# Kernel tuning notes

Measured on AMD Instinct MI355X. Metric: run time of the kernel, lower is better.

The kernel has to match this reference:

```python
import jax, jax.numpy as jnp
import numpy as np

B, S, D, NQ, NC, MC, K = 64, 200, 128, 50000, 1000, 4, 10
N = NQ + NC  # total graph nodes (concepts first, then questions, matching torch concat order)


def setup_inputs() -> dict:
    key = jax.random.key(0)
    ks = jax.random.split(key, 32)
    f = lambda i, shape: jax.random.normal(ks[i], shape, dtype=jnp.float32) * 0.02
    return {
        "emb_q": f(0, (NQ, D)), "emb_c": f(1, (NC, D)), "emb_r": f(2, (2, D)),
        "Wih1": f(3, (3 * D, 2 * D)), "Whh1": f(4, (3 * D, D)), "bih1": f(5, (3 * D,)), "bhh1": f(6, (3 * D,)),
        "Wih2": f(7, (3 * D, D)), "Whh2": f(8, (3 * D, D)), "bih2": f(9, (3 * D,)), "bhh2": f(10, (3 * D,)),
        "Wg1": f(11, (D, D)), "Wg2": f(12, (D, D)), "Wg3": f(13, (D, D)),
        "Wagg": f(14, (D, D)), "bagg": f(15, (D,)),
        "Wq": f(16, (D, D)), "bq": f(17, (D,)),
        "Wk": f(18, (D, D)), "bk": f(19, (D,)),
        "Ww": f(20, (1, 2 * D)), "bw": f(21, (1,)),
        "question_seq": jax.random.randint(ks[22], (B, S), 0, NQ),
        "correct_seq": jax.random.randint(ks[23], (B, S), 0, 2),
        "mask_seq": jnp.ones((B, S), dtype=jnp.int32),
        "q_table": jax.random.randint(ks[24], (NQ, MC), 0, NC),
    }


def _gru(x, h, Wih, Whh, bih, bhh):
    gi = x @ Wih.T + bih
    gh = h @ Whh.T + bhh
    i_r, i_z, i_n = jnp.split(gi, 3, axis=-1)
    h_r, h_z, h_n = jnp.split(gh, 3, axis=-1)
    r = jax.nn.sigmoid(i_r + h_r)
    z = jax.nn.sigmoid(i_z + h_z)
    n = jnp.tanh(i_n + r * h_n)
    return (1.0 - z) * n + z * h


def _sage_mean(x, src, dst, W):
    # SAGEConv4GIKT (eval): out = lin_r(mean_agg_over_neighbors + x), lin_r has no bias.
    agg = jax.ops.segment_sum(x[dst], src, num_segments=N)
    cnt = jax.ops.segment_sum(jnp.ones((src.shape[0], 1), x.dtype), src, num_segments=N)
    agg = agg / jnp.maximum(cnt, 1.0)
    return (agg + x) @ W.T


def reference(emb_q, emb_c, emb_r, Wih1, Whh1, bih1, bhh1, Wih2, Whh2, bih2, bhh2,
              Wg1, Wg2, Wg3, Wagg, bagg, Wq, bq, Wk, bk, Ww, bw,
              question_seq, correct_seq, mask_seq, q_table):
    # ---- GNN propagation over the full question-concept bipartite graph ----
    x = jnp.concatenate([emb_c, emb_q], axis=0)  # [N, D], concepts first
    q_glob = jnp.repeat(jnp.arange(NQ, dtype=q_table.dtype) + NC, MC)  # question global ids
    c_glob = q_table.reshape(-1)                                       # concept global ids
    x = _sage_mean(x, q_glob, c_glob, Wg1)  # q2c: aggregate at questions from concepts
    x = _sage_mean(x, c_glob, q_glob, Wg2)  # c2q: aggregate at concepts from questions
    x = _sage_mean(x, q_glob, c_glob, Wg3)  # q2c again
    x = jnp.tanh(x @ Wagg.T + bagg)

    tgrid = jnp.arange(S)

    def step(carry, inp):
        h1, h2, keyhist, statehist = carry
        t, q_t, r_t, m_t, q_next = inp
        m = (m_t != 0)[:, None]
        e_q = jnp.where(m, x[q_t + NC], emb_q[q_t])  # GNN emb where masked-in, raw emb otherwise
        e_r = emb_r[r_t]
        h1 = _gru(jnp.concatenate([e_q, e_r], axis=1), h1, Wih1, Whh1, bih1, bhh1)
        h2 = _gru(h1, h2, Wih2, Whh2, bih2, bhh2)
        statehist = statehist.at[:, t].set(h2)
        keyhist = keyhist.at[:, t].set(h2 @ Wk.T + bk)
        # queries: next question emb + its concept embs -> [B, MC+1, D]
        qc = jnp.concatenate([emb_q[q_next][:, None, :], emb_c[q_table[q_next]]], axis=1)
        aq = qc @ Wq.T + bq
        scores = jnp.einsum('bid,bjd->bij', aq, keyhist)  # [B, MC+1, S]
        scores = jnp.where((tgrid <= t)[None, None, :], scores, -1e9)
        flat = scores.reshape(B, -1)
        vals, idx = jax.lax.top_k(flat, K)  # top-k (query, state) pairs
        alpha = jax.nn.softmax(vals, axis=-1)
        i_idx = idx // S
        j_idx = idx % S
        q_sel = jnp.take_along_axis(qc, i_idx[:, :, None], axis=1)        # [B, K, D]
        s_sel = jnp.take_along_axis(statehist, j_idx[:, :, None], axis=1)  # [B, K, D]
        f = jax.nn.sigmoid(jnp.concatenate([q_sel, s_sel], axis=-1) @ Ww.T + bw)[..., 0]
        y = jnp.sum(alpha * f, axis=-1)  # [B]
        return (h1, h2, keyhist, statehist), y

    h0 = jnp.zeros((B, D), jnp.float32)
    carry = (h0, h0, jnp.zeros((B, S, D), jnp.float32), jnp.zeros((B, S, D), jnp.float32))
    xs = (jnp.arange(S - 1), question_seq[:, :-1].T, correct_seq[:, :-1].T,
          mask_seq[:, :-1].T, question_seq[:, 1:].T)
    _, ys = jax.lax.scan(step, carry, xs)
    y_hat = jnp.concatenate([jnp.zeros((B, 1), jnp.float32), ys.T], axis=1)  # predictions for t=1..S-1
    return y_hat
```

## Files before the change

kernel.cpp:

```cpp
#include <hip/hip_runtime.h>
#include <math.h>

#define Bz 64
#define Sz 200
#define Dz 128
#define NQz 50000
#define NCz 1000
#define MCz 4
#define Kz 10
#define Tz 199
#define NSz (Bz*Tz)
#define NEz (NQz*MCz)
#define KTpad 256

__global__ void k_count(const int* __restrict__ qt, int* __restrict__ cnt) {
    int e = blockIdx.x*256 + threadIdx.x;
    if (e < NEz) atomicAdd(&cnt[qt[e]], 1);
}

__global__ void k_offs(const int* __restrict__ cnt, int* __restrict__ offs) {
    __shared__ int s[1024];
    int tid = threadIdx.x;
    s[tid] = (tid < NCz) ? cnt[tid] : 0;
    __syncthreads();
    for (int off = 1; off < 1024; off <<= 1) {
        int add = (tid >= off) ? s[tid - off] : 0;
        __syncthreads();
        s[tid] += add;
        __syncthreads();
    }
    if (tid < NCz) offs[tid + 1] = s[tid];
    if (tid == 0) offs[0] = 0;
}

__global__ void k_fill(const int* __restrict__ qt, const int* __restrict__ offs,
                       int* __restrict__ fill, int* __restrict__ edge_q) {
    int e = blockIdx.x*256 + threadIdx.x;
    if (e < NEz) {
        int c = qt[e];
        int pos = atomicAdd(&fill[c], 1);
        edge_q[offs[c] + pos] = e >> 2;
    }
}

__global__ void k_m2(const int* __restrict__ qt, const int* __restrict__ offs,
                     const int* __restrict__ edge_q,
                     const float* __restrict__ emb_q, const float* __restrict__ emb_c,
                     float* __restrict__ m2) {
    int c = blockIdx.x;
    int g = threadIdx.x >> 7;
    int d = threadIdx.x & 127;
    int e0 = offs[c], e1 = offs[c+1];
    float acc = 0.f;
    for (int e = e0 + g; e < e1; e += 4) {
        int q = edge_q[e];
        const int* t4 = qt + q*4;
        int c0 = t4[0], c1 = t4[1], c2 = t4[2], c3 = t4[3];
        acc += emb_q[q*128 + d]
             + 0.25f*(emb_c[c0*128+d] + emb_c[c1*128+d] + emb_c[c2*128+d] + emb_c[c3*128+d]);
    }
    __shared__ float ps[4][128];
    ps[g][d] = acc;
    __syncthreads();
    if (g == 0) {
        float tot = ps[0][d] + ps[1][d] + ps[2][d] + ps[3][d];
        float cn = (float)(e1 - e0);
        m2[c*128 + d] = tot / fmaxf(cn, 1.0f);
    }
}

template<bool TR>
__global__ void k_mm128(const float* __restrict__ X, const float* __restrict__ Y,
                        float* __restrict__ out) {
    int r = blockIdx.x, c = threadIdx.x;
    float acc = 0.f;
    for (int e = 0; e < 128; ++e) acc += X[r*128 + e] * Y[e*128 + c];
    if (TR) out[c*128 + r] = acc;
    else    out[r*128 + c] = acc;
}

__global__ void k_gr(const float* __restrict__ emb_r, const float* __restrict__ Wih1,
                     const float* __restrict__ bih1, float* __restrict__ gr) {
    int rt = threadIdx.x / 384, r = threadIdx.x % 384;
    float acc = bih1[r];
    for (int e = 0; e < 128; ++e) acc += emb_r[rt*128 + e] * Wih1[r*256 + 128 + e];
    gr[rt*384 + r] = acc;
}

__global__ void k_bkq(const float* __restrict__ Wq, const float* __restrict__ Wk,
                      const float* __restrict__ bq, const float* __restrict__ bk,
                      const float* __restrict__ Ww, const float* __restrict__ bw,
                      float* __restrict__ Bkq, float* __restrict__ biaskq) {
    int r = blockIdx.x, d = threadIdx.x;
    if (r < 128) {
        float acc = 0.f;
        for (int n = 0; n < 128; ++n) acc += Wq[n*128 + r] * Wk[n*128 + d];
        Bkq[r*128 + d] = acc;
        if (d == 0) {
            float b0 = 0.f;
            for (int n = 0; n < 128; ++n) b0 += Wq[n*128 + r] * bk[n];
            biaskq[r] = b0;
        }
    } else if (r == 128) {
        float acc = 0.f;
        for (int n = 0; n < 128; ++n) acc += bq[n] * Wk[n*128 + d];
        Bkq[128*128 + d] = acc;
        if (d == 0) {
            float c0 = 0.f;
            for (int n = 0; n < 128; ++n) c0 += bq[n] * bk[n];
            biaskq[128] = c0;
        }
    } else {
        Bkq[129*128 + d] = Ww[128 + d];
        if (d == 0) biaskq[129] = bw[0];
    }
}

__global__ void k_eq(const float* __restrict__ Mt_g, const float* __restrict__ bagg,
                     const float* __restrict__ emb_q, const float* __restrict__ emb_c,
                     const float* __restrict__ m2, const int* __restrict__ qseq,
                     const int* __restrict__ mseq, const int* __restrict__ qt,
                     float* __restrict__ eq) {
    __shared__ float Mt[128*128];
    __shared__ float ub[2][128];
    int tid = threadIdx.x;
    for (int i = tid; i < 128*128/4; i += 256)
        ((float4*)Mt)[i] = ((const float4*)Mt_g)[i];
    __syncthreads();
    int g = tid >> 7, d = tid & 127;
    for (int it = 0; it < 8; ++it) {
        int slot = blockIdx.x*16 + it*2 + g;
        int b = slot / Tz, t = slot % Tz;
        int q = qseq[b*Sz + t];
        int msk = mseq[b*Sz + t];
        if (msk) {
            const int* t4 = qt + q*4;
            int c0 = t4[0], c1 = t4[1], c2 = t4[2], c3 = t4[3];
            ub[g][d] = emb_q[q*128 + d]
                     + 0.5f *(emb_c[c0*128+d] + emb_c[c1*128+d] + emb_c[c2*128+d] + emb_c[c3*128+d])
                     + 0.25f*(m2[c0*128+d]  + m2[c1*128+d]  + m2[c2*128+d]  + m2[c3*128+d]);
        }
        __syncthreads();
        if (msk) {
            float acc = bagg[d];
            const float* urow = ub[g];
            for (int e = 0; e < 128; ++e) acc += Mt[e*128 + d] * urow[e];
            eq[slot*128 + d] = tanhf(acc);
        } else {
            eq[slot*128 + d] = emb_q[q*128 + d];
        }
        __syncthreads();
    }
}

__device__ __forceinline__ float bf_lo(unsigned u){ return __uint_as_float(u << 16); }
__device__ __forceinline__ float bf_hi(unsigned u){ return __uint_as_float(u & 0xffff0000u); }
__device__ __forceinline__ unsigned f2bf(float x){
    unsigned u = __float_as_uint(x);
    return (u + 0x7fffu + ((u >> 16) & 1u)) >> 16;
}
__device__ __forceinline__ unsigned pk2(float a, float b){
    return f2bf(a) | (f2bf(b) << 16);
}
__device__ __forceinline__ float rcpf(float x){ return __builtin_amdgcn_rcpf(x); }
__device__ __forceinline__ float sigm(float x){ return rcpf(1.f + __expf(-x)); }
__device__ __forceinline__ float tanh_fast(float x){
    float e = __expf(2.f*x);
    return 1.f - 2.f*rcpf(e + 1.f);
}

#if __has_builtin(__builtin_amdgcn_fdot2_f32_bf16)
typedef __attribute__((ext_vector_type(2))) short short2v;
__device__ __forceinline__ float bdot2(unsigned w, unsigned h, float acc) {
    return __builtin_amdgcn_fdot2_f32_bf16(__builtin_bit_cast(short2v, w),
                                           __builtin_bit_cast(short2v, h), acc, false);
}
#else
__device__ __forceinline__ float bdot2(unsigned w, unsigned h, float acc) {
    return acc + bf_lo(w)*bf_lo(h) + bf_hi(w)*bf_hi(h);
}
#endif

typedef __attribute__((ext_vector_type(2))) float v2f;
__device__ __forceinline__ void pkfma_lo(v2f &acc, v2f k, v2f q) {
    asm("v_pk_fma_f32 %0, %1, %2, %0 op_sel_hi:[1,0,1]"
        : "+v"(acc) : "v"(k), "v"(q));
}
__device__ __forceinline__ void pkfma_hi(v2f &acc, v2f k, v2f q) {
    asm("v_pk_fma_f32 %0, %1, %2, %0 op_sel:[0,1,0] op_sel_hi:[1,1,1]"
        : "+v"(acc) : "v"(k), "v"(q));
}

template<int MODE, int DOT2>
__global__ void k_gemm(const float* __restrict__ A, const float* __restrict__ Bm,
                       int ldb, int nB, float* __restrict__ C, int ldc,
                       const float* __restrict__ bias, const float* __restrict__ gr,
                       const int* __restrict__ cseq) {
    __shared__ int rtb[64];
    int tx = threadIdx.x, ty = threadIdx.y;
    int tid = ty*16 + tx;
    int m0 = blockIdx.x * 64;
    int n0 = blockIdx.y * 64;
    if (MODE == 1 && tid < 64) {
        int s = m0 + tid;
        int b = s / Tz, t = s % Tz;
        rtb[tid] = cseq[b*Sz + t];
    }
    float acc[4][4];
    #pragma unroll
    for (int i = 0; i < 4; ++i)
        #pragma unroll
        for (int j = 0; j < 4; ++j) acc[i][j] = 0.f;

    if (DOT2) {
        __shared__ unsigned As[64][17];
        __shared__ unsigned Bs[64][17];
        for (int kc = 0; kc < 128; kc += 32) {
            #pragma unroll
            for (int l = 0; l < 2; ++l) {
                int v = tid*2 + l;
                int row = v >> 3, c4 = (v & 7) << 2;
                int p0 = (kc + c4) >> 1 & 15;
                float4 av = *(const float4*)(A + (size_t)(m0+row)*128 + kc + c4);
                As[row][p0]   = pk2(av.x, av.y);
                As[row][p0+1] = pk2(av.z, av.w);
                int nrow = n0 + row;
                float4 bv = make_float4(0.f, 0.f, 0.f, 0.f);
                if (nrow < nB) bv = *(const float4*)(Bm + (size_t)nrow*ldb + kc + c4);
                Bs[row][p0]   = pk2(bv.x, bv.y);
                Bs[row][p0+1] = pk2(bv.z, bv.w);
            }
            __syncthreads();
            #pragma unroll 4
            for (int kp = 0; kp < 16; ++kp) {
                unsigned av[4], bv[4];
                #pragma unroll
                for (int i = 0; i < 4; ++i) av[i] = As[ty*4+i][kp];
                #pragma unroll
                for (int j = 0; j < 4; ++j) bv[j] = Bs[tx*4+j][kp];
                #pragma unroll
                for (int i = 0; i < 4; ++i)
                    #pragma unroll
                    for (int j = 0; j < 4; ++j) acc[i][j] = bdot2(av[i], bv[j], acc[i][j]);
            }
            __syncthreads();
        }
    } else {
        __shared__ float Asf[64][33];
        __shared__ float Bsf[64][33];
        for (int kc = 0; kc < 128; kc += 32) {
            #pragma unroll
            for (int l = 0; l < 2; ++l) {
                int v = tid*2 + l;
                int row = v >> 3, c4 = (v & 7) << 2;
                float4 av = *(const float4*)(A + (size_t)(m0+row)*128 + kc + c4);
                Asf[row][c4+0] = av.x; Asf[row][c4+1] = av.y; Asf[row][c4+2] = av.z; Asf[row][c4+3] = av.w;
                int nrow = n0 + row;
                float4 bv = make_float4(0.f, 0.f, 0.f, 0.f);
                if (nrow < nB) bv = *(const float4*)(Bm + (size_t)nrow*ldb + kc + c4);
                Bsf[row][c4+0] = bv.x; Bsf[row][c4+1] = bv.y; Bsf[row][c4+2] = bv.z; Bsf[row][c4+3] = bv.w;
            }
            __syncthreads();
            #pragma unroll 8
            for (int k = 0; k < 32; ++k) {
                float av[4], bv[4];
                #pragma unroll
                for (int i = 0; i < 4; ++i) av[i] = Asf[ty*4+i][k];
                #pragma unroll
                for (int j = 0; j < 4; ++j) bv[j] = Bsf[tx*4+j][k];
                #pragma unroll
                for (int i = 0; i < 4; ++i)
                    #pragma unroll
                    for (int j = 0; j < 4; ++j) acc[i][j] += av[i]*bv[j];
            }
            __syncthreads();
        }
    }
    #pragma unroll
    for (int i = 0; i < 4; ++i) {
        int s = m0 + ty*4 + i;
        if (MODE == 2) {
            int bb = s / Tz, tt = s - ((int)(s / Tz))*Tz;
            #pragma unroll
            for (int j = 0; j < 4; ++j) {
                int col = n0 + tx*4 + j;
                if (col < nB)
                    C[((size_t)bb*132 + col)*KTpad + tt] = acc[i][j] + bias[col];
            }
        } else {
            #pragma unroll
            for (int j = 0; j < 4; ++j) {
                int col = n0 + tx*4 + j;
                if (col < nB) {
                    float v = acc[i][j];
                    if (MODE == 0) v += bias[col];
                    else           v += gr[rtb[ty*4+i]*384 + col];
                    C[(size_t)s*ldc + col] = v;
                }
            }
        }
    }
}

__global__ void __launch_bounds__(384, 1)
k_scan(const float* __restrict__ gi, const float* __restrict__ Whh,
       const float* __restrict__ bhh, float* __restrict__ hout) {
    int b0 = blockIdx.x*2, tid = threadIdx.x;

    unsigned w[64];
    {
        const float4* w4 = (const float4*)(Whh + (size_t)tid*128);
        #pragma unroll
        for (int k = 0; k < 32; ++k) {
            float4 v = w4[k];
            w[2*k] = pk2(v.x, v.y); w[2*k+1] = pk2(v.z, v.w);
        }
    }
    float bb = bhh[tid];

    __shared__ unsigned hb[2][64];
    __shared__ float gh[2][384];
    if (tid < 128) hb[tid>>6][tid&63] = 0u;

    float g0=0.f,g1=0.f,g2=0.f,g3=0.f,g4=0.f,g5=0.f;
    if (tid < 128) {
        const float2* gp = (const float2*)(gi + (size_t)((b0 + (tid>>6))*Tz)*384);
        int u = tid & 63;
        float2 x0 = gp[u], x1 = gp[u+64], x2 = gp[u+128];
        g0=x0.x; g1=x0.y; g2=x1.x; g3=x1.y; g4=x2.x; g5=x2.y;
    }
    __syncthreads();

    const uint4* hv0 = (const uint4*)hb[0];
    const uint4* hv1 = (const uint4*)hb[1];

    for (int t = 0; t < Tz; ++t) {
        float n0=0.f,n1=0.f,n2=0.f,n3=0.f,n4=0.f,n5=0.f;
        if (tid < 128 && t + 1 < Tz) {
            const float2* gp = (const float2*)(gi + (size_t)((b0 + (tid>>6))*Tz + t + 1)*384);
            int u = tid & 63;
            float2 x0 = gp[u], x1 = gp[u+64], x2 = gp[u+128];
            n0=x0.x; n1=x0.y; n2=x1.x; n3=x1.y; n4=x2.x; n5=x2.y;
        }
        float a0=0.f, a1=0.f, a2=0.f, a3=0.f;
        float c0=0.f, c1=0.f, c2=0.f, c3=0.f;
        #pragma unroll
        for (int k = 0; k < 8; ++k) {
            uint4 hp = hv0[k];
            uint4 hq = hv1[k];
            a0 = bdot2(w[4*k+0], hp.x, a0);
            a1 = bdot2(w[4*k+1], hp.y, a1);
            a2 = bdot2(w[4*k+2], hp.z, a2);
            a3 = bdot2(w[4*k+3], hp.w, a3);
            c0 = bdot2(w[4*k+0], hq.x, c0);
            c1 = bdot2(w[4*k+1], hq.y, c1);
            c2 = bdot2(w[4*k+2], hq.z, c2);
            c3 = bdot2(w[4*k+3], hq.w, c3);
        }
        gh[0][tid] = bb + ((a0+a1)+(a2+a3));
        gh[1][tid] = bb + ((c0+c1)+(c2+c3));
        __syncthreads();
        if (tid < 128) {
            int ch = tid >> 6;
            int u = 2*(tid & 63);
            unsigned hp = hb[ch][tid & 63];
            const float* ghc = gh[ch];
            float r0 = sigm(g0 + ghc[u]);
            float r1 = sigm(g1 + ghc[u+1]);
            float z0 = sigm(g2 + ghc[u+128]);
            float z1 = sigm(g3 + ghc[u+129]);
            float q0 = tanh_fast(g4 + r0*ghc[u+256]);
            float q1 = tanh_fast(g5 + r1*ghc[u+257]);
            float h0  = (1.f - z0)*q0 + z0*bf_lo(hp);
            float h1v = (1.f - z1)*q1 + z1*bf_hi(hp);
            hb[ch][tid & 63] = pk2(h0, h1v);
            ((float2*)(hout + (size_t)((b0+ch)*Tz + t)*128))[tid & 63] = make_float2(h0, h1v);
        }
        g0=n0; g1=n1; g2=n2; g3=n3; g4=n4; g5=n5;
        __syncthreads();
    }
}

__global__ void __launch_bounds__(256, 1)
k_attn(const float* __restrict__ kqt, const int* __restrict__ qseq,
       const int* __restrict__ qt, const float* __restrict__ emb_q,
       const float* __restrict__ emb_c, const float* __restrict__ Ww,
       float* __restrict__ out) {
    int wid  = threadIdx.x >> 6;
    int lane = threadIdx.x & 63;
    int b = blockIdx.y;
    int t = blockIdx.x*4 + wid;
    if (t > Tz - 1) t = Tz - 1;

    __shared__ float qc[4][5][128];
    __shared__ float gqs[4][5];
    int qn = qseq[b*Sz + t + 1];
    for (int idx = lane; idx < 5*128; idx += 64) {
        int i = idx / 128, d = idx & 127;
        const float* src = (i == 0) ? (emb_q + (size_t)qn*128)
                                    : (emb_c + (size_t)qt[qn*4 + (i-1)]*128);
        qc[wid][i][d] = src[d];
    }
    __syncthreads();
    {
        float w0 = Ww[lane], w1 = Ww[lane + 64];
        #pragma unroll
        for (int i = 0; i < 5; ++i) {
            float p = qc[wid][i][lane]*w0 + qc[wid][i][lane+64]*w1;
            #pragma unroll
            for (int off = 32; off >= 1; off >>= 1) p += __shfl_xor(p, off);
            if (lane == 0) gqs[wid][i] = p;
        }
    }
    __syncthreads();

    const float* base = kqt + (size_t)b*(132*KTpad);

    v2f accA[5], accB[5];
    #pragma unroll
    for (int i = 0; i < 5; ++i) { accA[i] = (v2f){0.f,0.f}; accB[i] = (v2f){0.f,0.f}; }

    #pragma unroll 2
    for (int c = 0; c < 32; ++c) {
        float4 k0 = ((const float4*)(base + (size_t)(4*c+0)*KTpad))[lane];
        float4 k1 = ((const float4*)(base + (size_t)(4*c+1)*KTpad))[lane];
        float4 k2 = ((const float4*)(base + (size_t)(4*c+2)*KTpad))[lane];
        float4 k3 = ((const float4*)(base + (size_t)(4*c+3)*KTpad))[lane];
        v2f k0a = {k0.x,k0.y}, k0b = {k0.z,k0.w};
        v2f k1a = {k1.x,k1.y}, k1b = {k1.z,k1.w};
        v2f k2a = {k2.x,k2.y}, k2b = {k2.z,k2.w};
        v2f k3a = {k3.x,k3.y}, k3b = {k3.z,k3.w};
        #pragma unroll
        for (int i = 0; i < 5; ++i) {
            float4 q = ((const float4*)qc[wid][i])[c];
            v2f qa = {q.x,q.y}, qb = {q.z,q.w};
            pkfma_lo(accA[i], k0a, qa); pkfma_lo(accB[i], k0b, qa);
            pkfma_hi(accA[i], k1a, qa); pkfma_hi(accB[i], k1b, qa);
            pkfma_lo(accA[i], k2a, qb); pkfma_lo(accB[i], k2b, qb);
            pkfma_hi(accA[i], k3a, qb); pkfma_hi(accB[i], k3b, qb);
        }
    }

    const float NEG = -3.402823466e38f;
    float sv[10]; int si[10];
    #pragma unroll
    for (int k = 0; k < 10; ++k) { sv[k] = NEG; si[k] = 0x7FFFFFFF; }

    auto ins = [&](float cv, int ci) {
        if (cv > sv[9] || (cv == sv[9] && ci < si[9])) {
            #pragma unroll
            for (int k = 0; k < 10; ++k) {
                bool bet = (cv > sv[k]) || (cv == sv[k] && ci < si[k]);
                float tv = sv[k]; int ti = si[k];
                if (bet) { sv[k] = cv; si[k] = ci; cv = tv; ci = ti; }
            }
        }
    };
    {
        float4 kb4 = ((const float4*)(base + 128*KTpad))[lane];
        float kbv[4] = {kb4.x, kb4.y, kb4.z, kb4.w};
        #pragma unroll
        for (int jj = 0; jj < 4; ++jj) {
            int j = 4*lane + jj;
            if (j <= t) {
                #pragma unroll
                for (int i = 0; i < 5; ++i) {
                    float a = (jj == 0) ? accA[i].x : (jj == 1) ? accA[i].y
                            : (jj == 2) ? accB[i].x : accB[i].y;
                    ins(a + kbv[jj], i*Sz + j);
                }
            }
        }
    }

    float vmax = 0.f, myv = 0.f; int myidx = 0x7FFFFFFF;
    #pragma unroll
    for (int rnd = 0; rnd < 10; ++rnd) {
        float v = sv[0]; int idx = si[0];
        #pragma unroll
        for (int off = 32; off >= 1; off >>= 1) {
            float ov = __shfl_xor(v, off);
            int   oi = __shfl_xor(idx, off);
            if (ov > v || (ov == v && oi < idx)) { v = ov; idx = oi; }
        }
        if (rnd == 0) vmax = v;
        if (lane == rnd) { myv = v; myidx = idx; }
        if (si[0] == idx) {
            #pragma unroll
            for (int k = 0; k < 9; ++k) { sv[k] = sv[k+1]; si[k] = si[k+1]; }
            sv[9] = NEG; si[9] = 0x7FFFFFFF;
        }
    }

    float num = 0.f, den = 0.f;
    if (lane < 10 && myidx != 0x7FFFFFFF) {
        float a = __expf(myv - vmax);
        int ik = myidx / Sz, jk = myidx % Sz;
        float gsj = base[129*KTpad + jk];
        float f = sigm(gqs[wid][ik] + gsj);
        num = a*f; den = a;
    }
    #pragma unroll
    for (int off = 32; off >= 1; off >>= 1) {
        num += __shfl_xor(num, off);
        den += __shfl_xor(den, off);
    }
    if (lane == 0) out[b*Sz + t + 1] = num/den;
}

static inline size_t alup(size_t x) { return (x + 255) & ~(size_t)255; }

extern "C" void kernel_launch(void* const* d_in, const int* in_sizes, int n_in,
                              void* d_out, int out_size, void* d_ws, size_t ws_size,
                              hipStream_t stream) {
    (void)in_sizes; (void)n_in; (void)ws_size;
    const float* emb_q = (const float*)d_in[0];
    const float* emb_c = (const float*)d_in[1];
    const float* emb_r = (const float*)d_in[2];
    const float* Wih1  = (const float*)d_in[3];
    const float* Whh1  = (const float*)d_in[4];
    const float* bih1  = (const float*)d_in[5];
    const float* bhh1  = (const float*)d_in[6];
    const float* Wih2  = (const float*)d_in[7];
    const float* Whh2  = (const float*)d_in[8];
    const float* bih2  = (const float*)d_in[9];
    const float* bhh2  = (const float*)d_in[10];
    const float* Wg1   = (const float*)d_in[11];
    const float* Wg2   = (const float*)d_in[12];
    const float* Wg3   = (const float*)d_in[13];
    const float* Wagg  = (const float*)d_in[14];
    const float* bagg  = (const float*)d_in[15];
    const float* Wq    = (const float*)d_in[16];
    const float* bq    = (const float*)d_in[17];
    const float* Wk    = (const float*)d_in[18];
    const float* bk    = (const float*)d_in[19];
    const float* Ww    = (const float*)d_in[20];
    const float* bw    = (const float*)d_in[21];
    const int* qseq    = (const int*)d_in[22];
    const int* cseq    = (const int*)d_in[23];
    const int* mseq    = (const int*)d_in[24];
    const int* qtab    = (const int*)d_in[25];
    float* out = (float*)d_out;

    char* p = (char*)d_ws;
    auto alloc = [&](size_t bytes) { char* r = p; p += alup(bytes); return r; };
    int*   cnt    = (int*)  alloc(4096);
    int*   fill   = (int*)  alloc(4096);
    int*   offs   = (int*)  alloc(1001*4);
    int*   edge_q = (int*)  alloc((size_t)NEz*4);
    float* m2     = (float*)alloc((size_t)NCz*128*4);
    float* T1     = (float*)alloc(128*128*4);
    float* T2     = (float*)alloc(128*128*4);
    float* Mt     = (float*)alloc(128*128*4);
    float* gr     = (float*)alloc(2*384*4);
    float* Bkq    = (float*)alloc(132*128*4);
    float* biaskq = (float*)alloc(132*4);
    float* eq     = (float*)alloc((size_t)NSz*128*4);
    float* gi1    = (float*)alloc((size_t)NSz*384*4);
    float* stateh = (float*)alloc((size_t)NSz*128*4);
    float* kqt    = (float*)alloc((size_t)Bz*132*KTpad*4);
    float* h1all = eq;
    float* gi2   = gi1;

    hipMemsetAsync(cnt, 0, 8192, stream);
    hipMemsetAsync(d_out, 0, (size_t)out_size*4, stream);

    k_count<<<(NEz+255)/256, 256, 0, stream>>>(qtab, cnt);
    k_offs <<<1, 1024, 0, stream>>>(cnt, offs);
    k_fill <<<(NEz+255)/256, 256, 0, stream>>>(qtab, offs, fill, edge_q);
    k_m2   <<<NCz, 512, 0, stream>>>(qtab, offs, edge_q, emb_q, emb_c, m2);

    k_mm128<false><<<128, 128, 0, stream>>>(Wg2, Wg1, T1);
    k_mm128<false><<<128, 128, 0, stream>>>(Wg3, T1, T2);
    k_mm128<true> <<<128, 128, 0, stream>>>(Wagg, T2, Mt);
    k_gr  <<<1, 768, 0, stream>>>(emb_r, Wih1, bih1, gr);
    k_bkq <<<130, 128, 0, stream>>>(Wq, Wk, bq, bk, Ww, bw, Bkq, biaskq);

    k_eq  <<<NSz/16, 256, 0, stream>>>(Mt, bagg, emb_q, emb_c, m2, qseq, mseq, qtab, eq);

    k_gemm<1,1><<<dim3(NSz/64, 6), dim3(16,16), 0, stream>>>(eq, Wih1, 256, 384,
                                                             gi1, 384, nullptr, gr, cseq);
    k_scan<<<Bz/2, 384, 0, stream>>>(gi1, Whh1, bhh1, h1all);
    k_gemm<0,1><<<dim3(NSz/64, 6), dim3(16,16), 0, stream>>>(h1all, Wih2, 128, 384,
                                                             gi2, 384, bih2, nullptr, nullptr);
    k_scan<<<Bz/2, 384, 0, stream>>>(gi2, Whh2, bhh2, stateh);

    k_gemm<2,0><<<dim3(NSz/64, 3), dim3(16,16), 0, stream>>>(stateh, Bkq, 128, 132,
                                                             kqt, 0, biaskq, nullptr, nullptr);
    k_attn<<<dim3((Tz+3)/4, Bz), 256, 0, stream>>>(kqt, qseq, qtab, emb_q, emb_c, Ww, out);
}
```

Baseline: 718.9 us.

## Restructure GRU scan to one batch per block with split-K shuffle reduction

After: 695.3 us. 3.3% less time.

```diff
diff --git a/kernel.cpp b/kernel.cpp
--- a/kernel.cpp
+++ b/kernel.cpp
@@ -302,81 +302,97 @@
     }
 }
 
-__global__ void __launch_bounds__(384, 1)
+__global__ void __launch_bounds__(512, 1)
 k_scan(const float* __restrict__ gi, const float* __restrict__ Whh,
        const float* __restrict__ bhh, float* __restrict__ hout) {
-    int b0 = blockIdx.x*2, tid = threadIdx.x;
-
-    unsigned w[64];
+    int b = blockIdx.x, tid = threadIdx.x;
+    int wid = tid >> 6, lane = tid & 63;
+    int u  = wid*16 + (lane & 15);
+    int qh = lane >> 4;
+
+    unsigned wr[16], wz[16], wn[16];
     {
-        const float4* w4 = (const float4*)(Whh + (size_t)tid*128);
-        #pragma unroll
-        for (int k = 0; k < 32; ++k) {
-            float4 v = w4[k];
-            w[2*k] = pk2(v.x, v.y); w[2*k+1] = pk2(v.z, v.w);
-        }
-    }
-    float bb = bhh[tid];
-
-    __shared__ unsigned hb[2][64];
-    __shared__ float gh[2][384];
-    if (tid < 128) hb[tid>>6][tid&63] = 0u;
-
-    float g0=0.f,g1=0.f,g2=0.f,g3=0.f,g4=0.f,g5=0.f;
-    if (tid < 128) {
-        const float2* gp = (const float2*)(gi + (size_t)((b0 + (tid>>6))*Tz)*384);
-        int u = tid & 63;
-        float2 x0 = gp[u], x1 = gp[u+64], x2 = gp[u+128];
-        g0=x0.x; g1=x0.y; g2=x1.x; g3=x1.y; g4=x2.x; g5=x2.y;
-    }
-    __syncthreads();
-
-    const uint4* hv0 = (const uint4*)hb[0];
-    const uint4* hv1 = (const uint4*)hb[1];
-
-    for (int t = 0; t < Tz; ++t) {
-        float n0=0.f,n1=0.f,n2=0.f,n3=0.f,n4=0.f,n5=0.f;
-        if (tid < 128 && t + 1 < Tz) {
-            const float2* gp = (const float2*)(gi + (size_t)((b0 + (tid>>6))*Tz + t + 1)*384);
-            int u = tid & 63;
-            float2 x0 = gp[u], x1 = gp[u+64], x2 = gp[u+128];
-            n0=x0.x; n1=x0.y; n2=x1.x; n3=x1.y; n4=x2.x; n5=x2.y;
-        }
-        float a0=0.f, a1=0.f, a2=0.f, a3=0.f;
-        float c0=0.f, c1=0.f, c2=0.f, c3=0.f;
+        const float4* r4 = (const float4*)(Whh + (size_t)u*128       + qh*32);
+        const float4* z4 = (const float4*)(Whh + (size_t)(u+128)*128 + qh*32);
+        const float4* n4 = (const float4*)(Whh + (size_t)(u+256)*128 + qh*32);
         #pragma unroll
         for (int k = 0; k < 8; ++k) {
-            uint4 hp = hv0[k];
-            uint4 hq = hv1[k];
-            a0 = bdot2(w[4*k+0], hp.x, a0);
-            a1 = bdot2(w[4*k+1], hp.y, a1);
-            a2 = bdot2(w[4*k+2], hp.z, a2);
-            a3 = bdot2(w[4*k+3], hp.w, a3);
-            c0 = bdot2(w[4*k+0], hq.x, c0);
-            c1 = bdot2(w[4*k+1], hq.y, c1);
-            c2 = bdot2(w[4*k+2], hq.z, c2);
-            c3 = bdot2(w[4*k+3], hq.w, c3);
-        }
-        gh[0][tid] = bb + ((a0+a1)+(a2+a3));
-        gh[1][tid] = bb + ((c0+c1)+(c2+c3));
-        __syncthreads();
-        if (tid < 128) {
-            int ch = tid >> 6;
-            int u = 2*(tid & 63);
-            unsigned hp = hb[ch][tid & 63];
-            const float* ghc = gh[ch];
-            float r0 = sigm(g0 + ghc[u]);
-            float r1 = sigm(g1 + ghc[u+1]);
-            float z0 = sigm(g2 + ghc[u+128]);
-            float z1 = sigm(g3 + ghc[u+129]);
-            float q0 = tanh_fast(g4 + r0*ghc[u+256]);
-            float q1 = tanh_fast(g5 + r1*ghc[u+257]);
-            float h0  = (1.f - z0)*q0 + z0*bf_lo(hp);
-            float h1v = (1.f - z1)*q1 + z1*bf_hi(hp);
-            hb[ch][tid & 63] = pk2(h0, h1v);
-            ((float2*)(hout + (size_t)((b0+ch)*Tz + t)*128))[tid & 63] = make_float2(h0, h1v);
-        }
-        g0=n0; g1=n1; g2=n2; g3=n3; g4=n4; g5=n5;
+            float4 a = r4[k]; wr[2*k] = pk2(a.x, a.y); wr[2*k+1] = pk2(a.z, a.w);
+            float4 c = z4[k]; wz[2*k] = pk2(c.x, c.y); wz[2*k+1] = pk2(c.z, c.w);
+            float4 d = n4[k]; wn[2*k] = pk2(d.x, d.y); wn[2*k+1] = pk2(d.z, d.w);
+        }
+    }
+    float br = bhh[u], bz = bhh[u+128], bn = bhh[u+256];
+
+    __shared__ unsigned hb[2][64];
+    if (tid < 64) { hb[0][tid] = 0u; hb[1][tid] = 0u; }
+    float hold = 0.f;
+
+    const float* gbase = gi + (size_t)(b*Tz)*384;
+    float gc0 = gbase[u], gc1 = gbase[u+128], gc2 = gbase[u+256];
+    float ga0 = gbase[384+u], ga1 = gbase[384+u+128], ga2 = gbase[384+u+256];
+    __syncthreads();
+
+    for (int t = 0; t < Tz; ++t) {
+        float gm0 = 0.f, gm1 = 0.f, gm2 = 0.f;
+        if (t + 2 < Tz) {
+            const float* gp = gbase + (size_t)(t+2)*384;
+            gm0 = gp[u]; gm1 = gp[u+128]; gm2 = gp[u+256];
+        }
+        const unsigned* hc = hb[t & 1];
+        const uint4* hv = (const uint4*)(hc + qh*16);
+        uint4 h0 = hv[0], h1 = hv[1], h2 = hv[2], h3 = hv[3];
+        float ar, az, an;
+        {
+            float p0=0.f, p1=0.f;
+            p0 = bdot2(wr[0],  h0.x, p0); p1 = bdot2(wr[1],  h0.y, p1);
+            p0 = bdot2(wr[2],  h0.z, p0); p1 = bdot2(wr[3],  h0.w, p1);
+            p0 = bdot2(wr[4],  h1.x, p0); p1 = bdot2(wr[5],  h1.y, p1);
+            p0 = bdot2(wr[6],  h1.z, p0); p1 = bdot2(wr[7],  h1.w, p1);
+            p0 = bdot2(wr[8],  h2.x, p0); p1 = bdot2(wr[9],  h2.y, p1);
+            p0 = bdot2(wr[10], h2.z, p0); p1 = bdot2(wr[11], h2.w, p1);
+            p0 = bdot2(wr[12], h3.x, p0); p1 = bdot2(wr[13], h3.y, p1);
+            p0 = bdot2(wr[14], h3.z, p0); p1 = bdot2(wr[15], h3.w, p1);
+            ar = p0 + p1;
+        }
+        {
+            float p0=0.f, p1=0.f;
+            p0 = bdot2(wz[0],  h0.x, p0); p1 = bdot2(wz[1],  h0.y, p1);
+            p0 = bdot2(wz[2],  h0.z, p0); p1 = bdot2(wz[3],  h0.w, p1);
+            p0 = bdot2(wz[4],  h1.x, p0); p1 = bdot2(wz[5],  h1.y, p1);
+            p0 = bdot2(wz[6],  h1.z, p0); p1 = bdot2(wz[7],  h1.w, p1);
+            p0 = bdot2(wz[8],  h2.x, p0); p1 = bdot2(wz[9],  h2.y, p1);
+            p0 = bdot2(wz[10], h2.z, p0); p1 = bdot2(wz[11], h2.w, p1);
+            p0 = bdot2(wz[12], h3.x, p0); p1 = bdot2(wz[13], h3.y, p1);
+            p0 = bdot2(wz[14], h3.z, p0); p1 = bdot2(wz[15], h3.w, p1);
+            az = p0 + p1;
+        }
+        {
+            float p0=0.f, p1=0.f;
+            p0 = bdot2(wn[0],  h0.x, p0); p1 = bdot2(wn[1],  h0.y, p1);
+            p0 = bdot2(wn[2],  h0.z, p0); p1 = bdot2(wn[3],  h0.w, p1);
+            p0 = bdot2(wn[4],  h1.x, p0); p1 = bdot2(wn[5],  h1.y, p1);
+            p0 = bdot2(wn[6],  h1.z, p0); p1 = bdot2(wn[7],  h1.w, p1);
+            p0 = bdot2(wn[8],  h2.x, p0); p1 = bdot2(wn[9],  h2.y, p1);
+            p0 = bdot2(wn[10], h2.z, p0); p1 = bdot2(wn[11], h2.w, p1);
+            p0 = bdot2(wn[12], h3.x, p0); p1 = bdot2(wn[13], h3.y, p1);
+            p0 = bdot2(wn[14], h3.z, p0); p1 = bdot2(wn[15], h3.w, p1);
+            an = p0 + p1;
+        }
+        ar += __shfl_xor(ar, 16); ar += __shfl_xor(ar, 32);
+        az += __shfl_xor(az, 16); az += __shfl_xor(az, 32);
+        an += __shfl_xor(an, 16); an += __shfl_xor(an, 32);
+        float rr = sigm(gc0 + br + ar);
+        float zz = sigm(gc1 + bz + az);
+        float nn = tanh_fast(gc2 + rr*(bn + an));
+        float hnew = (1.f - zz)*nn + zz*hold;
+        hold = hnew;
+        if (qh == 0) {
+            ((unsigned short*)hb[(t & 1) ^ 1])[u] = (unsigned short)f2bf(hnew);
+            hout[(size_t)(b*Tz + t)*128 + u] = hnew;
+        }
+        gc0 = ga0; gc1 = ga1; gc2 = ga2;
+        ga0 = gm0; ga1 = gm1; ga2 = gm2;
         __syncthreads();
     }
 }
@@ -580,10 +596,10 @@
 
     k_gemm<1,1><<<dim3(NSz/64, 6), dim3(16,16), 0, stream>>>(eq, Wih1, 256, 384,
                                                              gi1, 384, nullptr, gr, cseq);
-    k_scan<<<Bz/2, 384, 0, stream>>>(gi1, Whh1, bhh1, h1all);
+    k_scan<<<Bz, 512, 0, stream>>>(gi1, Whh1, bhh1, h1all);
     k_gemm<0,1><<<dim3(NSz/64, 6), dim3(16,16), 0, stream>>>(h1all, Wih2, 128, 384,
                                                              gi2, 384, bih2, nullptr, nullptr);
-    k_scan<<<Bz/2, 384, 0, stream>>>(gi2, Whh2, bhh2, stateh);
+    k_scan<<<Bz, 512, 0, stream>>>(gi2, Whh2, bhh2, stateh);
 
     k_gemm<2,0><<<dim3(NSz/64, 3), dim3(16,16), 0, stream>>>(stateh, Bkq, 128, 132,
                                                              kqt, 0, biaskq, nullptr, nullptr);
```
